# Performance work log

Hardware: AMD Instinct MI355X
Metric: run time of the kernel (lower is better)

The kernel has to match this reference:

```python
import jax, jax.numpy as jnp
import numpy as np

HEADS = 16
HEAD_DIM = 128


def rotate_half(x):
    x1, x2 = jnp.split(x, 2, axis=-1)
    return jnp.concatenate((-x2, x1), axis=-1)


def setup_inputs() -> dict:
    key = jax.random.key(0)
    ks = jax.random.split(key, 8)
    b, s, h = 2, 2048, 2048
    x = jax.random.normal(ks[0], (b, s, h), dtype=jnp.float32)
    attention_mask = jnp.zeros((1, 1, s, s), dtype=jnp.float32)
    alibi = jax.random.normal(ks[1], (1, HEADS, 1, s), dtype=jnp.float32)
    freqs = jax.random.normal(ks[2], (1, 1, s, HEAD_DIM), dtype=jnp.float32)
    scale = 1.0 / np.sqrt(h)
    Wq = jax.random.normal(ks[3], (h, h), dtype=jnp.float32) * scale
    Wk = jax.random.normal(ks[4], (h, h), dtype=jnp.float32) * scale
    Wv = jax.random.normal(ks[5], (h, h), dtype=jnp.float32) * scale
    Wo = jax.random.normal(ks[6], (h, h), dtype=jnp.float32) * scale
    return {"x": x, "attention_mask": attention_mask, "alibi": alibi,
            "freqs": freqs, "Wq": Wq, "Wk": Wk, "Wv": Wv, "Wo": Wo}


def reference(x, attention_mask, alibi, freqs, Wq, Wk, Wv, Wo):
    b, s, hidden = x.shape
    # torch Linear: y = x @ W.T (weight shape [out, in])
    def proj(W):
        y = x @ W.T
        return y.reshape(b, s, HEADS, HEAD_DIM).transpose(0, 2, 1, 3)  # [b,H,s,d]
    q, k, v = proj(Wq), proj(Wk), proj(Wv)
    cos, sin = jnp.cos(freqs), jnp.sin(freqs)
    q = q * cos + rotate_half(q) * sin
    k = k * cos + rotate_half(k) * sin
    scores = jnp.einsum('bhqd,bhkd->bhqk', q, k) / np.sqrt(HEAD_DIM)
    scores = scores + attention_mask + alibi
    attn = jax.nn.softmax(scores, axis=-1)
    out = jnp.einsum('bhqk,bhkd->bhqd', attn, v)
    out = out.transpose(0, 2, 1, 3).reshape(b, s, hidden)
    return out @ Wo.T
```

## Files before the change

kernel.cpp:

```cpp
#include <hip/hip_runtime.h>
#include <math.h>

typedef __attribute__((ext_vector_type(8))) short short8;
typedef __attribute__((ext_vector_type(4))) float f32x4;
typedef __attribute__((ext_vector_type(4))) unsigned short us4;
typedef __attribute__((ext_vector_type(4))) float fl4;

#define B_ 2
#define S_ 2048
#define H_ 16
#define D_ 128
#define HID 2048

__device__ __forceinline__ unsigned short f2bf(float f){
  unsigned u = __builtin_bit_cast(unsigned, f);
  u += 0x7fffu + ((u >> 16) & 1u);
  return (unsigned short)(u >> 16);
}
__device__ __forceinline__ float bf2f(unsigned short u){
  unsigned x = ((unsigned)u) << 16;
  return __builtin_bit_cast(float, x);
}
__device__ __forceinline__ int cvtpk(float lo, float hi){
  int r; asm("v_cvt_pk_bf16_f32 %0, %1, %2" : "=v"(r) : "v"(lo), "v"(hi)); return r;
}

__device__ __forceinline__ void g2lds16(const unsigned short* g, unsigned short* l){
  __builtin_amdgcn_global_load_lds(
      (const __attribute__((address_space(1))) unsigned int*)g,
      (__attribute__((address_space(3))) unsigned int*)l, 16, 0, 0);
}

__global__ void cvt_k(const float* __restrict__ src, unsigned short* __restrict__ dst){
  int i = (blockIdx.x * 256 + threadIdx.x) * 4;
  fl4 v = *(const fl4*)(src + i);
  us4 o;
  #pragma unroll
  for (int t = 0; t < 4; t++) o[t] = f2bf(v[t]);
  *(us4*)(dst + i) = o;
}

__global__ void tab_k(const float* __restrict__ freqs, float* __restrict__ ctab,
                      float* __restrict__ stab){
  int i = blockIdx.x * 256 + threadIdx.x;
  float f = freqs[i];
  ctab[i] = cosf(f);
  stab[i] = sinf(f);
}

#define SB __builtin_amdgcn_sched_barrier(0)
#define BAR __builtin_amdgcn_s_barrier()
#define VM(n) asm volatile("s_waitcnt vmcnt(" #n ")" ::: "memory")

#define RD_A8(slotb, half) do { _Pragma("unroll") \
  for (int i = 0; i < 4; i++){ _Pragma("unroll") \
    for (int ks = 0; ks < 2; ks++) \
      a[i][ks] = *(const short8*)(L + (slotb) + (half)*8192 + abase + i*2048 + kg[ks]); } } while(0)

#define RD_B8(slotb) do { _Pragma("unroll") \
  for (int n = 0; n < 2; n++){ _Pragma("unroll") \
    for (int ks = 0; ks < 2; ks++) \
      b[n][ks] = *(const short8*)(L + (slotb) + 16384 + bbase + n*4096 + kg[ks]); } } while(0)

#define MMQ8(X) do { __builtin_amdgcn_s_setprio(1); _Pragma("unroll") \
  for (int i = 0; i < 4; i++){ _Pragma("unroll") \
    for (int n = 0; n < 2; n++){ _Pragma("unroll") \
      for (int ks = 0; ks < 2; ks++) \
        acc[(X)*4+i][n] = __builtin_amdgcn_mfma_f32_16x16x32_bf16( \
            a[i][ks], b[n][ks], acc[(X)*4+i][n], 0, 0, 0); } } \
  __builtin_amdgcn_s_setprio(0); } while(0)

template<int EPI>
__global__ __launch_bounds__(512, 2) void gemm8_k(
    const unsigned short* __restrict__ A,
    const unsigned short* __restrict__ W0,
    const unsigned short* __restrict__ W1,
    const unsigned short* __restrict__ W2,
    unsigned short* __restrict__ O0,
    unsigned short* __restrict__ O1,
    unsigned short* __restrict__ O2,
    float* __restrict__ Of)
{
  __shared__ __align__(16) unsigned short L[2 * 3 * 8192];
  const int tid = threadIdx.x;
  const int l = tid & 63, lg = l >> 4, lr = l & 15;
  const int w = tid >> 6, wm = w >> 2, wn = w & 3;
  const int m0 = blockIdx.x * 256, n0 = blockIdx.y * 128;
  const int z = (EPI == 1) ? blockIdx.z : 0;
  const unsigned short* Bop = (EPI == 1) ? (z == 0 ? W0 : (z == 1 ? W1 : W2)) : W0;

  f32x4 acc[8][2];
  #pragma unroll
  for (int i = 0; i < 8; i++)
    #pragma unroll
    for (int j = 0; j < 2; j++)
      acc[i][j] = f32x4{0.f, 0.f, 0.f, 0.f};

  const int gsw = (((tid & 7) ^ ((tid >> 3) & 7)) * 8);
  const unsigned short* gA = A   + (size_t)(m0 + (tid >> 3)) * HID + gsw;
  const unsigned short* gB = Bop + (size_t)(n0 + (tid >> 3)) * HID + gsw;
  const size_t HIN = (size_t)64  * HID;
  const size_t HB  = (size_t)128 * HID;

  const int abase = (wm * 16 + lr) * 64;
  const int bbase = (wn * 16 + lr) * 64;
  int kg[2];
  kg[0] = ((lg)     ^ (lr & 7)) * 8;
  kg[1] = ((4 + lg) ^ (lr & 7)) * 8;

  #define STG(gsrc, tile, ldst) do { \
    const unsigned short* _s = (gsrc) + (size_t)(tile) * 64; \
    g2lds16(_s,       (ldst) + tid * 8); \
    g2lds16(_s + HIN, (ldst) + 4096 + tid * 8); } while(0)

  short8 a[4][2], b[2][2];

  STG(gA,      0, L);
  STG(gA + HB, 0, L + 8192);
  STG(gB,      0, L + 16384);
  VM(0); SB; BAR;

  #define PH1(sl, osl, tn) do { \
    RD_A8(sl, 0); RD_B8(sl); \
    STG(gA, tn, L + (osl)); STG(gB, tn, L + (osl) + 16384); \
    BAR; MMQ8(0); VM(4); SB; BAR; } while(0)
  #define PH2(sl, osl, tn) do { \
    RD_A8(sl, 1); \
    STG(gA + HB, tn, L + (osl) + 8192); \
    BAR; MMQ8(1); VM(2); SB; BAR; } while(0)

  for (int it = 0; it < 15; ++it){
    const int t1 = 2 * it + 1, t2 = 2 * it + 2;
    PH1(0, 24576, t1); PH2(0, 24576, t1);
    PH1(24576, 0, t2); PH2(24576, 0, t2);
  }
  PH1(0, 24576, 31); PH2(0, 24576, 31);
  RD_A8(24576, 0); RD_B8(24576);
  BAR; MMQ8(0); VM(0); SB; BAR;
  RD_A8(24576, 1);
  BAR; MMQ8(1);
  #undef PH1
  #undef PH2
  #undef STG

  #pragma unroll
  for (int mf = 0; mf < 8; mf++)
    #pragma unroll
    for (int nf = 0; nf < 2; nf++){
      const int j = n0 + nf * 64 + wn * 16 + lr;
      const int i0 = m0 + mf * 32 + wm * 16 + lg * 4;
      if (EPI == 0){
        #pragma unroll
        for (int r = 0; r < 4; r++)
          Of[(size_t)(i0 + r) * HID + j] = acc[mf][nf][r];
      } else if (z == 2){
        const int b = i0 >> 11, s = i0 & 2047, h = j >> 7, d = j & 127;
        us4 v;
        #pragma unroll
        for (int r = 0; r < 4; r++) v[r] = f2bf(acc[mf][nf][r]);
        *(us4*)(O2 + ((size_t)(b * H_ + h) * D_ + d) * S_ + s) = v;
      } else {
        unsigned short* O = z ? O1 : O0;
        const int h = j >> 7, d = j & 127;
        #pragma unroll
        for (int r = 0; r < 4; r++){
          const int i = i0 + r;
          const int b = i >> 11, s = i & 2047;
          O[((size_t)(b * H_ + h) * S_ + s) * D_ + d] = f2bf(acc[mf][nf][r]);
        }
      }
    }
}

__global__ void rope_k(unsigned short* __restrict__ Q, unsigned short* __restrict__ K,
                       const float* __restrict__ ctab, const float* __restrict__ stab){
  int idx = blockIdx.x * 256 + threadIdx.x;
  unsigned short* P = (idx >= (1 << 20)) ? K : Q;
  int e  = idx & ((1 << 20) - 1);
  int g  = e & 15;
  int s  = (e >> 4) & 2047;
  int bh = e >> 15;
  int d0 = g * 4;
  size_t base = ((size_t)bh * S_ + s) * D_;
  us4 qa = *(us4*)(P + base + d0);
  us4 qb = *(us4*)(P + base + d0 + 64);
  fl4 ca = *(const fl4*)(ctab + s * D_ + d0);
  fl4 sa = *(const fl4*)(stab + s * D_ + d0);
  fl4 cb = *(const fl4*)(ctab + s * D_ + d0 + 64);
  fl4 sb = *(const fl4*)(stab + s * D_ + d0 + 64);
  us4 oa, ob;
  #pragma unroll
  for (int t = 0; t < 4; t++){
    float xa = bf2f(qa[t]), xb = bf2f(qb[t]);
    oa[t] = f2bf(xa * ca[t] - xb * sa[t]);
    ob[t] = f2bf(xb * cb[t] + xa * sb[t]);
  }
  *(us4*)(P + base + d0)      = oa;
  *(us4*)(P + base + d0 + 64) = ob;
}

__global__ __launch_bounds__(256) void attn_k(
    const unsigned short* __restrict__ Q,
    const unsigned short* __restrict__ Kg,
    const unsigned short* __restrict__ Vt,
    const float* __restrict__ mask,
    const float* __restrict__ alibi,
    unsigned short* __restrict__ Ctx)
{
  __shared__ __align__(16) unsigned short Kl[2][64 * 128];
  __shared__ __align__(16) unsigned short Vl[2][128 * 64];
  const int tid = threadIdx.x;
  const int l = tid & 63, lg = l >> 4, lr = l & 15;
  const int w = tid >> 6;
  const int bh = blockIdx.y, b = bh >> 4, h = bh & 15;
  const int q0 = blockIdx.x * 64 + w * 16;
  const size_t hb = (size_t)bh * S_ * D_;
  const float* mrow = mask + (size_t)(q0 + lr) * S_;
  const float* al = alibi + h * S_;
  const int sidx = (l & 48) + ((l & 48) >> 2);
  const float SCL2E = 0.08838834764831845f * 1.4426950408889634f;
  const float L2E = 1.4426950408889634f;

  const int kswz = (((tid & 15) ^ ((tid >> 4) & 7)) * 8);
  const unsigned short* gK = Kg + hb + (size_t)(tid >> 4) * D_ + kswz;
  const int vswz = (((tid & 7) ^ ((tid >> 3) & 7)) * 8);
  const unsigned short* gV = Vt + hb + (size_t)(tid >> 3) * S_ + vswz;

  #define ASTAGE(buf, kv)  do {                                            \
    g2lds16(gK + (size_t)((kv))      * D_, Kl[buf] + tid * 8);             \
    g2lds16(gK + (size_t)((kv) + 16) * D_, Kl[buf] + 2048 + tid * 8);      \
    g2lds16(gK + (size_t)((kv) + 32) * D_, Kl[buf] + 4096 + tid * 8);      \
    g2lds16(gK + (size_t)((kv) + 48) * D_, Kl[buf] + 6144 + tid * 8);      \
    g2lds16(gV + (kv),                     Vl[buf] + tid * 8);             \
    g2lds16(gV + 32 * S_ + (kv),           Vl[buf] + 2048 + tid * 8);      \
    g2lds16(gV + 64 * S_ + (kv),           Vl[buf] + 4096 + tid * 8);      \
    g2lds16(gV + 96 * S_ + (kv),           Vl[buf] + 6144 + tid * 8);      \
  } while (0)

  int koff[4];
  #pragma unroll
  for (int c = 0; c < 4; c++) koff[c] = ((c * 4 + lg) ^ (lr & 7)) * 8;
  const int vo0 = (lg ^ (lr & 7)) * 8, vo1 = ((4 + lg) ^ (lr & 7)) * 8;

  short8 qf[4];
  #pragma unroll
  for (int c = 0; c < 4; c++)
    qf[c] = *(const short8*)(Q + hb + (size_t)(q0 + lr) * D_ + c * 32 + lg * 8);

  f32x4 acc[8];
  #pragma unroll
  for (int c = 0; c < 8; c++) acc[c] = f32x4{0.f, 0.f, 0.f, 0.f};
  float mr = -1e30f, lsum = 0.f;

  ASTAGE(0, 0);
  __syncthreads();
  int cur = 0;

  for (int t = 0; t < 32; t++){
    const int kv0 = t * 64;
    if (t < 31) ASTAGE(cur ^ 1, kv0 + 64);

    fl4 mk[4], aa[4];
    #pragma unroll
    for (int g = 0; g < 4; g++){
      mk[g] = *(const fl4*)(mrow + kv0 + g * 16 + 4 * lg);
      aa[g] = *(const fl4*)(al  + kv0 + g * 16 + 4 * lg);
    }

    f32x4 sg[4];
    #pragma unroll
    for (int g = 0; g < 4; g++) sg[g] = f32x4{0.f, 0.f, 0.f, 0.f};
    #pragma unroll
    for (int g = 0; g < 4; g++){
      const int row = g * 16 + lr;
      #pragma unroll
      for (int c = 0; c < 4; c++){
        short8 kf = *(const short8*)(Kl[cur] + row * 128 + koff[c]);
        sg[g] = __builtin_amdgcn_mfma_f32_16x16x32_bf16(kf, qf[c], sg[g], 0, 0, 0);
      }
    }

    float x[4][4];
    #pragma unroll
    for (int g = 0; g < 4; g++)
      #pragma unroll
      for (int r = 0; r < 4; r++)
        x[g][r] = fmaf(sg[g][r], SCL2E, (mk[g][r] + aa[g][r]) * L2E);

    float mx = -1e30f;
    #pragma unroll
    for (int g = 0; g < 4; g++)
      #pragma unroll
      for (int r = 0; r < 4; r++) mx = fmaxf(mx, x[g][r]);

    float p[4][4], ps = 0.f;
    if (__all(mx <= mr + 8.f)){
      #pragma unroll
      for (int g = 0; g < 4; g++)
        #pragma unroll
        for (int r = 0; r < 4; r++){
          p[g][r] = exp2f(x[g][r] - mr);
          ps += p[g][r];
        }
      ps += __shfl_xor(ps, 16);
      ps += __shfl_xor(ps, 32);
      lsum += ps;
    } else {
      mx = fmaxf(mx, __shfl_xor(mx, 16));
      mx = fmaxf(mx, __shfl_xor(mx, 32));
      float mnew = fmaxf(mr, mx);
      float alpha = exp2f(mr - mnew);
      #pragma unroll
      for (int g = 0; g < 4; g++)
        #pragma unroll
        for (int r = 0; r < 4; r++){
          p[g][r] = exp2f(x[g][r] - mnew);
          ps += p[g][r];
        }
      ps += __shfl_xor(ps, 16);
      ps += __shfl_xor(ps, 32);
      lsum = lsum * alpha + ps;
      mr = mnew;
      float ar[4];
      #pragma unroll
      for (int r = 0; r < 4; r++) ar[r] = __shfl(alpha, sidx + r);
      #pragma unroll
      for (int c = 0; c < 8; c++)
        #pragma unroll
        for (int r = 0; r < 4; r++) acc[c][r] *= ar[r];
    }

    int pk0[4], pk1[4];
    #pragma unroll
    for (int r = 0; r < 4; r++){
      pk0[r] = cvtpk(p[0][r], p[1][r]);
      pk1[r] = cvtpk(p[2][r], p[3][r]);
    }

    const int srcb = lr + ((lg & 1) << 5);
    short8 af0, af1;
    #pragma unroll
    for (int j = 0; j < 8; j++){
      int w0 = __shfl(pk0[j & 3], srcb + ((j >> 2) << 4));
      int w1 = __shfl(pk1[j & 3], srcb + ((j >> 2) << 4));
      af0[j] = (short)((l & 32) ? ((unsigned)w0 >> 16) : ((unsigned)w0 & 0xffffu));
      af1[j] = (short)((l & 32) ? ((unsigned)w1 >> 16) : ((unsigned)w1 & 0xffffu));
    }

    #pragma unroll
    for (int c = 0; c < 8; c++){
      const int d0 = c * 16 + lr;
      short8 vf0 = *(const short8*)(Vl[cur] + d0 * 64 + vo0);
      short8 vf1 = *(const short8*)(Vl[cur] + d0 * 64 + vo1);
      acc[c] = __builtin_amdgcn_mfma_f32_16x16x32_bf16(af0, vf0, acc[c], 0, 0, 0);
      acc[c] = __builtin_amdgcn_mfma_f32_16x16x32_bf16(af1, vf1, acc[c], 0, 0, 0);
    }

    __syncthreads();
    cur ^= 1;
  }
  #undef ASTAGE

  float inv = 1.f / lsum;
  float ir[4];
  #pragma unroll
  for (int r = 0; r < 4; r++) ir[r] = __shfl(inv, sidx + r);
  #pragma unroll
  for (int r = 0; r < 4; r++){
    const int qg = q0 + 4 * lg + r;
    const size_t ob = ((size_t)(b * S_ + qg) * H_ + h) * D_;
    #pragma unroll
    for (int c = 0; c < 8; c++)
      Ctx[ob + c * 16 + lr] = f2bf(acc[c][r] * ir[r]);
  }
}

extern "C" void kernel_launch(void* const* d_in, const int* in_sizes, int n_in,
                              void* d_out, int out_size, void* d_ws, size_t ws_size,
                              hipStream_t stream){
  const float* x     = (const float*)d_in[0];
  const float* mask  = (const float*)d_in[1];
  const float* alibi = (const float*)d_in[2];
  const float* freqs = (const float*)d_in[3];
  const float* Wq    = (const float*)d_in[4];
  const float* Wk    = (const float*)d_in[5];
  const float* Wv    = (const float*)d_in[6];
  const float* Wo    = (const float*)d_in[7];
  float* out = (float*)d_out;

  unsigned short* ws  = (unsigned short*)d_ws;
  unsigned short* xb  = ws;
  unsigned short* wqb = ws + 8388608;
  unsigned short* wkb = ws + 12582912;
  unsigned short* wvb = ws + 16777216;
  unsigned short* wob = ws + 20971520;
  unsigned short* Qb  = ws + 25165824;
  unsigned short* Kb  = ws + 33554432;
  unsigned short* Vb  = ws + 41943040;
  unsigned short* ctx = xb;
  float* ctab = (float*)(ws + 50331648);
  float* stab = ctab + 262144;

  cvt_k<<<8192, 256, 0, stream>>>(x,  xb);
  cvt_k<<<4096, 256, 0, stream>>>(Wq, wqb);
  cvt_k<<<4096, 256, 0, stream>>>(Wk, wkb);
  cvt_k<<<4096, 256, 0, stream>>>(Wv, wvb);
  cvt_k<<<4096, 256, 0, stream>>>(Wo, wob);
  tab_k<<<1024, 256, 0, stream>>>(freqs, ctab, stab);

  gemm8_k<1><<<dim3(16, 16, 3), 512, 0, stream>>>(xb, wqb, wkb, wvb,
                                                  Qb, Kb, Vb, nullptr);
  rope_k<<<8192, 256, 0, stream>>>(Qb, Kb, ctab, stab);
  attn_k<<<dim3(32, 32), 256, 0, stream>>>(Qb, Kb, Vb, mask, alibi, ctx);
  gemm8_k<0><<<dim3(16, 16, 1), 512, 0, stream>>>(ctx, wob, nullptr, nullptr,
                                                  nullptr, nullptr, nullptr, out);
}
```

Measured before the change: 498.8 us.

## Fuse RoPE into QKV GEMM epilogue, merge weight casts, remap attention grid

```diff
diff --git a/kernel.cpp b/kernel.cpp
--- a/kernel.cpp
+++ b/kernel.cpp
@@ -38,6 +38,20 @@
   #pragma unroll
   for (int t = 0; t < 4; t++) o[t] = f2bf(v[t]);
   *(us4*)(dst + i) = o;
+}
+
+__global__ void cvtw_k(const float* __restrict__ Wq, const float* __restrict__ Wk,
+                       const float* __restrict__ Wv, const float* __restrict__ Wo,
+                       unsigned short* __restrict__ dst){
+  int bi = blockIdx.x;
+  int which = bi >> 12;
+  const float* src = which == 0 ? Wq : (which == 1 ? Wk : (which == 2 ? Wv : Wo));
+  int local = ((bi & 4095) * 256 + threadIdx.x) * 4;
+  fl4 v = *(const fl4*)(src + local);
+  us4 o;
+  #pragma unroll
+  for (int t = 0; t < 4; t++) o[t] = f2bf(v[t]);
+  *(us4*)(dst + which * 4194304 + local) = o;
 }
 
 __global__ void tab_k(const float* __restrict__ freqs, float* __restrict__ ctab,
@@ -79,7 +93,9 @@
     unsigned short* __restrict__ O0,
     unsigned short* __restrict__ O1,
     unsigned short* __restrict__ O2,
-    float* __restrict__ Of)
+    float* __restrict__ Of,
+    const float* __restrict__ ctab,
+    const float* __restrict__ stab)
 {
   __shared__ __align__(16) unsigned short L[2 * 3 * 8192];
   const int tid = threadIdx.x;
@@ -143,60 +159,49 @@
   #undef PH2
   #undef STG
 
-  #pragma unroll
-  for (int mf = 0; mf < 8; mf++)
-    #pragma unroll
-    for (int nf = 0; nf < 2; nf++){
-      const int j = n0 + nf * 64 + wn * 16 + lr;
-      const int i0 = m0 + mf * 32 + wm * 16 + lg * 4;
-      if (EPI == 0){
+  if (EPI == 0){
+    #pragma unroll
+    for (int mf = 0; mf < 8; mf++)
+      #pragma unroll
+      for (int nf = 0; nf < 2; nf++){
+        const int j = n0 + nf * 64 + wn * 16 + lr;
+        const int i0 = m0 + mf * 32 + wm * 16 + lg * 4;
         #pragma unroll
         for (int r = 0; r < 4; r++)
           Of[(size_t)(i0 + r) * HID + j] = acc[mf][nf][r];
-      } else if (z == 2){
+      }
+  } else if (z == 2){
+    #pragma unroll
+    for (int mf = 0; mf < 8; mf++)
+      #pragma unroll
+      for (int nf = 0; nf < 2; nf++){
+        const int j = n0 + nf * 64 + wn * 16 + lr;
+        const int i0 = m0 + mf * 32 + wm * 16 + lg * 4;
         const int b = i0 >> 11, s = i0 & 2047, h = j >> 7, d = j & 127;
         us4 v;
         #pragma unroll
         for (int r = 0; r < 4; r++) v[r] = f2bf(acc[mf][nf][r]);
         *(us4*)(O2 + ((size_t)(b * H_ + h) * D_ + d) * S_ + s) = v;
-      } else {
-        unsigned short* O = z ? O1 : O0;
-        const int h = j >> 7, d = j & 127;
-        #pragma unroll
-        for (int r = 0; r < 4; r++){
-          const int i = i0 + r;
-          const int b = i >> 11, s = i & 2047;
-          O[((size_t)(b * H_ + h) * S_ + s) * D_ + d] = f2bf(acc[mf][nf][r]);
-        }
       }
-    }
-}
-
-__global__ void rope_k(unsigned short* __restrict__ Q, unsigned short* __restrict__ K,
-                       const float* __restrict__ ctab, const float* __restrict__ stab){
-  int idx = blockIdx.x * 256 + threadIdx.x;
-  unsigned short* P = (idx >= (1 << 20)) ? K : Q;
-  int e  = idx & ((1 << 20) - 1);
-  int g  = e & 15;
-  int s  = (e >> 4) & 2047;
-  int bh = e >> 15;
-  int d0 = g * 4;
-  size_t base = ((size_t)bh * S_ + s) * D_;
-  us4 qa = *(us4*)(P + base + d0);
-  us4 qb = *(us4*)(P + base + d0 + 64);
-  fl4 ca = *(const fl4*)(ctab + s * D_ + d0);
-  fl4 sa = *(const fl4*)(stab + s * D_ + d0);
-  fl4 cb = *(const fl4*)(ctab + s * D_ + d0 + 64);
-  fl4 sb = *(const fl4*)(stab + s * D_ + d0 + 64);
-  us4 oa, ob;
-  #pragma unroll
-  for (int t = 0; t < 4; t++){
-    float xa = bf2f(qa[t]), xb = bf2f(qb[t]);
-    oa[t] = f2bf(xa * ca[t] - xb * sa[t]);
-    ob[t] = f2bf(xb * cb[t] + xa * sb[t]);
+  } else {
+    unsigned short* O = z ? O1 : O0;
+    const int h = n0 >> 7;
+    const int dlo = wn * 16 + lr;
+    #pragma unroll
+    for (int mf = 0; mf < 8; mf++){
+      #pragma unroll
+      for (int r = 0; r < 4; r++){
+        const int i = m0 + mf * 32 + wm * 16 + lg * 4 + r;
+        const int b = i >> 11, s = i & 2047;
+        const float xa = acc[mf][0][r], xb = acc[mf][1][r];
+        const float cl = ctab[s * D_ + dlo],      sl = stab[s * D_ + dlo];
+        const float ch = ctab[s * D_ + dlo + 64], sh = stab[s * D_ + dlo + 64];
+        const size_t base = ((size_t)(b * H_ + h) * S_ + s) * D_;
+        O[base + dlo]      = f2bf(xa * cl - xb * sl);
+        O[base + dlo + 64] = f2bf(xb * ch + xa * sh);
+      }
+    }
   }
-  *(us4*)(P + base + d0)      = oa;
-  *(us4*)(P + base + d0 + 64) = ob;
 }
 
 __global__ __launch_bounds__(256) void attn_k(
@@ -212,8 +217,11 @@
   const int tid = threadIdx.x;
   const int l = tid & 63, lg = l >> 4, lr = l & 15;
   const int w = tid >> 6;
-  const int bh = blockIdx.y, b = bh >> 4, h = bh & 15;
-  const int q0 = blockIdx.x * 64 + w * 16;
+  const int f = blockIdx.x;
+  const int g0 = (f & 7) * 128 + (f >> 3);
+  const int bh = g0 >> 5, qx = g0 & 31;
+  const int b = bh >> 4, h = bh & 15;
+  const int q0 = qx * 64 + w * 16;
   const size_t hb = (size_t)bh * S_ * D_;
   const float* mrow = mask + (size_t)(q0 + lr) * S_;
   const float* al = alibi + h * S_;
@@ -401,17 +409,14 @@
   float* ctab = (float*)(ws + 50331648);
   float* stab = ctab + 262144;
 
-  cvt_k<<<8192, 256, 0, stream>>>(x,  xb);
-  cvt_k<<<4096, 256, 0, stream>>>(Wq, wqb);
-  cvt_k<<<4096, 256, 0, stream>>>(Wk, wkb);
-  cvt_k<<<4096, 256, 0, stream>>>(Wv, wvb);
-  cvt_k<<<4096, 256, 0, stream>>>(Wo, wob);
   tab_k<<<1024, 256, 0, stream>>>(freqs, ctab, stab);
+  cvt_k<<<8192, 256, 0, stream>>>(x, xb);
+  cvtw_k<<<16384, 256, 0, stream>>>(Wq, Wk, Wv, Wo, wqb);
 
   gemm8_k<1><<<dim3(16, 16, 3), 512, 0, stream>>>(xb, wqb, wkb, wvb,
-                                                  Qb, Kb, Vb, nullptr);
-  rope_k<<<8192, 256, 0, stream>>>(Qb, Kb, ctab, stab);
-  attn_k<<<dim3(32, 32), 256, 0, stream>>>(Qb, Kb, Vb, mask, alibi, ctx);
+                                                  Qb, Kb, Vb, nullptr, ctab, stab);
+  attn_k<<<1024, 256, 0, stream>>>(Qb, Kb, Vb, mask, alibi, ctx);
   gemm8_k<0><<<dim3(16, 16, 1), 512, 0, stream>>>(ctx, wob, nullptr, nullptr,
-                                                  nullptr, nullptr, nullptr, out);
-}
+                                                  nullptr, nullptr, nullptr, out,
+                                                  nullptr, nullptr);
+}
```

After: 463.4 us. -7.1%, faster.
